# Optimization experiments

Measured on AMD Instinct MI355X. Metric: run time of the kernel, lower is better.

Reference implementation:

```python
import jax, jax.numpy as jnp
import numpy as np

TIME_LAG, PRE_LEN, STATIONS, SAMPLES = 12, 3, 40, 38
B, H, DM, DFF = 4, 8, 512, 2048
L = STATIONS * SAMPLES          # 1520 tokens fed to Informer
SAMPLE_K = 40                   # factor(5)*ceil(ln L); also n_top selected queries
N_ENC = 2


def sinusoid(length, d):
    pos = np.arange(length, dtype=np.float32)[:, None]
    i = np.arange(d)[None, :]
    ang = pos / np.power(10000.0, (2 * (i // 2)) / d)
    pe = np.where(i % 2 == 0, np.sin(ang), np.cos(ang)).astype(np.float32)
    return jnp.asarray(pe)


def layernorm(x, g, b, eps=1e-5):
    mu = x.mean(-1, keepdims=True)
    var = ((x - mu) ** 2).mean(-1, keepdims=True)
    return (x - mu) * jax.lax.rsqrt(var + eps) * g + b


def heads(x):
    b, l, d = x.shape
    return x.reshape(b, l, H, d // H).transpose(0, 2, 1, 3)


def unheads(x):
    b, h, l, dh = x.shape
    return x.transpose(0, 2, 1, 3).reshape(b, l, h * dh)


def prob_attention(Q, K, V, idx):
    # ProbSparse attention (Informer). Q,K,V: [B,H,L,Dh]; idx: [L, SAMPLE_K] sampled key ids.
    b, h, l, dh = Q.shape
    def col(ic):  # one sampled key per query; avoids [B,H,L,S,Dh] gather blowup
        return jnp.einsum('bhld,bhld->bhl', Q, K[:, :, ic, :])
    qk_s = jnp.moveaxis(jax.lax.map(col, idx.T), 0, -1)       # [B,H,L,SAMPLE_K]
    M = qk_s.max(-1) - qk_s.sum(-1) / l                        # sparsity measure
    _, top = jax.lax.top_k(M, SAMPLE_K)                        # [B,H,n_top]
    Qr = jnp.take_along_axis(Q, top[..., None], axis=2)        # [B,H,n_top,Dh]
    scores = jnp.einsum('bhud,bhkd->bhuk', Qr, K) / jnp.sqrt(jnp.float32(dh))
    ctx_top = jax.nn.softmax(scores, axis=-1) @ V              # [B,H,n_top,Dh]
    ctx = jnp.broadcast_to(V.mean(axis=2, keepdims=True), Q.shape)
    bi = jnp.arange(b)[:, None, None]
    hi = jnp.arange(h)[None, :, None]
    return ctx.at[bi, hi, top].set(ctx_top)


def full_attention(Q, K, V):
    scores = jnp.einsum('bhqd,bhkd->bhqk', Q, K) / jnp.sqrt(jnp.float32(Q.shape[-1]))
    return jax.nn.softmax(scores, axis=-1) @ V


def ffn(x, Wa, ba, Wb, bb):
    return jax.nn.gelu(x @ Wa + ba) @ Wb + bb


def _forward(inflow, P, samp_idx):
    x = inflow[:, 2:2 + TIME_LAG].reshape(B, -1, TIME_LAG)     # [B,L,T] (row-major, same as torch)
    pe = sinusoid(L, DM)
    enc = x @ P['W_emb_e'] + P['b_emb_e'] + pe
    for i in range(N_ENC):
        qkv = enc @ P['enc_Wqkv'][i] + P['enc_bqkv'][i]
        q, k, v = jnp.split(qkv, 3, axis=-1)
        ctx = unheads(prob_attention(heads(q), heads(k), heads(v), samp_idx[i]))
        enc = layernorm(enc + ctx @ P['enc_Wo'][i] + P['enc_bo'][i], P['enc_ln1_g'][i], P['enc_ln1_b'][i])
        y = ffn(enc, P['enc_Wf1'][i], P['enc_bf1'][i], P['enc_Wf2'][i], P['enc_bf2'][i])
        enc = layernorm(enc + y, P['enc_ln2_g'][i], P['enc_ln2_b'][i])
    enc = layernorm(enc, P['enc_norm_g'], P['enc_norm_b'])
    dec = x @ P['W_emb_d'] + P['b_emb_d'] + pe
    qkv = dec @ P['dec_Wqkv'] + P['dec_bqkv']
    q, k, v = jnp.split(qkv, 3, axis=-1)
    ctx = unheads(prob_attention(heads(q), heads(k), heads(v), samp_idx[2]))
    dec = layernorm(dec + ctx @ P['dec_Wo_s'] + P['dec_bo_s'], P['dec_ln1_g'], P['dec_ln1_b'])
    qc = dec @ P['dec_Wq_c'] + P['dec_bq_c']
    kc, vc = jnp.split(enc @ P['dec_Wkv_c'] + P['dec_bkv_c'], 2, axis=-1)
    ctx = unheads(full_attention(heads(qc), heads(kc), heads(vc)))
    dec = layernorm(dec + ctx @ P['dec_Wo_c'] + P['dec_bo_c'], P['dec_ln2_g'], P['dec_ln2_b'])
    y = ffn(dec, P['dec_Wf1'], P['dec_bf1'], P['dec_Wf2'], P['dec_bf2'])
    dec = layernorm(dec + y, P['dec_ln3_g'], P['dec_ln3_b'])
    out = dec @ P['W_proj'] + P['b_proj'] + x                  # Informer output + residual
    out = jax.nn.relu(out @ P['W1'] + P['b1']) @ P['W3'] + P['b3']
    return out.reshape(B, PRE_LEN, STATIONS, SAMPLES)


def setup_inputs():
    key = jax.random.key(0)
    keys = iter(jax.random.split(key, 80))
    def w(*shape):
        return jax.random.normal(next(keys), shape, jnp.float32) * 0.02
    def zeros(*shape):
        return jnp.zeros(shape, jnp.float32)
    def ones(*shape):
        return jnp.ones(shape, jnp.float32)
    inp = dict(
        flow=zeros(1), ODRate=zeros(1), adj=zeros(1), external=zeros(1),
        inflow=jax.random.normal(next(keys), (B, 2 + TIME_LAG, STATIONS, SAMPLES), jnp.float32),
        W_emb_e=w(TIME_LAG, DM), b_emb_e=zeros(DM),
        W_emb_d=w(TIME_LAG, DM), b_emb_d=zeros(DM),
        enc_Wqkv=w(N_ENC, DM, 3 * DM), enc_bqkv=zeros(N_ENC, 3 * DM),
        enc_Wo=w(N_ENC, DM, DM), enc_bo=zeros(N_ENC, DM),
        enc_ln1_g=ones(N_ENC, DM), enc_ln1_b=zeros(N_ENC, DM),
        enc_Wf1=w(N_ENC, DM, DFF), enc_bf1=zeros(N_ENC, DFF),
        enc_Wf2=w(N_ENC, DFF, DM), enc_bf2=zeros(N_ENC, DM),
        enc_ln2_g=ones(N_ENC, DM), enc_ln2_b=zeros(N_ENC, DM),
        enc_norm_g=ones(DM), enc_norm_b=zeros(DM),
        dec_Wqkv=w(DM, 3 * DM), dec_bqkv=zeros(3 * DM),
        dec_Wo_s=w(DM, DM), dec_bo_s=zeros(DM),
        dec_ln1_g=ones(DM), dec_ln1_b=zeros(DM),
        dec_Wq_c=w(DM, DM), dec_bq_c=zeros(DM),
        dec_Wkv_c=w(DM, 2 * DM), dec_bkv_c=zeros(2 * DM),
        dec_Wo_c=w(DM, DM), dec_bo_c=zeros(DM),
        dec_ln2_g=ones(DM), dec_ln2_b=zeros(DM),
        dec_Wf1=w(DM, DFF), dec_bf1=zeros(DFF),
        dec_Wf2=w(DFF, DM), dec_bf2=zeros(DM),
        dec_ln3_g=ones(DM), dec_ln3_b=zeros(DM),
        W_proj=w(DM, TIME_LAG), b_proj=zeros(TIME_LAG),
        W1=w(TIME_LAG, 128), b1=zeros(128),
        W3=w(128, PRE_LEN), b3=zeros(PRE_LEN),
        samp_idx=jax.random.randint(next(keys), (3, L, SAMPLE_K), 0, L, jnp.int32),
    )
    return inp


def reference(flow, inflow, ODRate, adj, external, W_emb_e, b_emb_e, W_emb_d, b_emb_d, enc_Wqkv, enc_bqkv, enc_Wo, enc_bo, enc_ln1_g, enc_ln1_b, enc_Wf1, enc_bf1, enc_Wf2, enc_bf2, enc_ln2_g, enc_ln2_b, enc_norm_g, enc_norm_b, dec_Wqkv, dec_bqkv, dec_Wo_s, dec_bo_s, dec_ln1_g, dec_ln1_b, dec_Wq_c, dec_bq_c, dec_Wkv_c, dec_bkv_c, dec_Wo_c, dec_bo_c, dec_ln2_g, dec_ln2_b, dec_Wf1, dec_bf1, dec_Wf2, dec_bf2, dec_ln3_g, dec_ln3_b, W_proj, b_proj, W1, b1, W3, b3, samp_idx):
    args = locals()
    skip = ('flow', 'inflow', 'ODRate', 'adj', 'external', 'samp_idx')
    P = {k: v for k, v in args.items() if k not in skip}
    return _forward(inflow, P, samp_idx)
```

## Files before the change

kernel.cpp:

```cpp
#include <hip/hip_runtime.h>
#include <math.h>

#define B_ 4
#define H_ 8
#define L_ 1520
#define DM_ 512
#define DFF_ 2048
#define SK_ 40
#define ML_ (B_*L_)
#define MP_ 6144
#define LP_ 1536

typedef unsigned short u16;
typedef short s8v __attribute__((ext_vector_type(8)));
typedef float f4 __attribute__((ext_vector_type(4)));

__device__ __forceinline__ u16 f2b(float x) {
  union { float f; unsigned u; } c; c.f = x;
  unsigned r = c.u + 0x7FFFu + ((c.u >> 16) & 1u);
  return (u16)(r >> 16);
}
__device__ __forceinline__ float b2f(u16 h) {
  union { unsigned u; float f; } c; c.u = ((unsigned)h) << 16;
  return c.f;
}
__device__ __forceinline__ float gelu_tanh(float x) {
  float x3 = x * x * x;
  return 0.5f * x * (1.f + tanhf(0.79788456080286536f * (x + 0.044715f * x3)));
}
__device__ __forceinline__ int xswz(int bid, int cpx) {
  return (bid & 7) * cpx + (bid >> 3);
}

__global__ __launch_bounds__(256) void pe_kernel(float* __restrict__ pe) {
  int idx = blockIdx.x * 256 + threadIdx.x;
  if (idx >= L_ * DM_) return;
  int pos = idx / DM_, i = idx % DM_;
  double expo = (double)(2 * (i / 2)) / (double)DM_;
  double ang = (double)pos / pow(10000.0, expo);
  pe[idx] = (i & 1) ? (float)cos(ang) : (float)sin(ang);
}

__global__ __launch_bounds__(256) void extract_x(const float* __restrict__ inflow,
                                                 float* __restrict__ X) {
  int idx = blockIdx.x * 256 + threadIdx.x;
  if (idx >= ML_ * 12) return;
  int b = idx / (L_ * 12);
  int rem = idx - b * (L_ * 12);
  X[idx] = inflow[(size_t)b * 14 * L_ + 2 * L_ + rem];
}

struct CvtArgs {
  const float* src[15];
  unsigned cum[16];
  unsigned lk[15];
};
__global__ __launch_bounds__(256) void cvt_all(CvtArgs a, u16* __restrict__ dst) {
  unsigned idx = blockIdx.x * 256 + threadIdx.x;
  int s = 0;
#pragma unroll
  for (int i = 1; i < 15; ++i) s += (idx >= a.cum[i]);
  unsigned local = idx - a.cum[s];
  unsigned lk = a.lk[s];
  unsigned K = 1u << lk;
  unsigned N = (a.cum[s + 1] - a.cum[s]) >> lk;
  unsigned n = local >> lk, k = local & (K - 1);
  dst[idx] = f2b(a.src[s][(size_t)k * N + n]);
}

__global__ __launch_bounds__(256) void embed_fused(
    const float* __restrict__ X, const float* __restrict__ W,
    const float* __restrict__ bias, const float* __restrict__ PE,
    float* __restrict__ ACT, u16* __restrict__ ACTb) {
  int row = blockIdx.x * 4 + (threadIdx.x >> 6);
  int lane = threadIdx.x & 63;
  int d0 = lane * 8;
  if (row >= ML_) {
    s8v z = {0, 0, 0, 0, 0, 0, 0, 0};
    *(s8v*)(ACTb + (size_t)row * DM_ + d0) = z;
    return;
  }
  int prow = row % L_;
  f4 a0 = *(const f4*)(bias + d0);
  f4 a1 = *(const f4*)(bias + d0 + 4);
  a0 += *(const f4*)(PE + (size_t)prow * DM_ + d0);
  a1 += *(const f4*)(PE + (size_t)prow * DM_ + d0 + 4);
  const float* xr = X + (size_t)row * 12;
#pragma unroll
  for (int t = 0; t < 12; ++t) {
    float xv = xr[t];
    a0 += xv * *(const f4*)(W + (size_t)t * DM_ + d0);
    a1 += xv * *(const f4*)(W + (size_t)t * DM_ + d0 + 4);
  }
  float* dst = ACT + (size_t)row * DM_ + d0;
  *(f4*)dst = a0;
  *(f4*)(dst + 4) = a1;
  u16 ob[8];
#pragma unroll
  for (int i = 0; i < 4; ++i) { ob[i] = f2b(a0[i]); ob[4 + i] = f2b(a1[i]); }
  *(s8v*)(ACTb + (size_t)row * DM_ + d0) = *(s8v*)ob;
}

__global__ __launch_bounds__(256) void head_fused(
    const float* __restrict__ DEC, const float* __restrict__ X,
    const float* __restrict__ Wp, const float* __restrict__ bp,
    const float* __restrict__ W1, const float* __restrict__ b1,
    const float* __restrict__ W3, const float* __restrict__ b3,
    float* __restrict__ out) {
  int row = blockIdx.x * 4 + (threadIdx.x >> 6);
  int lane = threadIdx.x & 63;
  int d0 = lane * 8;
  const float* dec = DEC + (size_t)row * DM_ + d0;
  f4 v0 = *(const f4*)dec;
  f4 v1 = *(const f4*)(dec + 4);
  float pj[12];
#pragma unroll
  for (int j = 0; j < 12; ++j) pj[j] = 0.f;
#pragma unroll
  for (int i = 0; i < 8; ++i) {
    float dv = (i < 4) ? v0[i] : v1[i - 4];
    const float* wr = Wp + (size_t)(d0 + i) * 12;
#pragma unroll
    for (int j = 0; j < 12; ++j) pj[j] += dv * wr[j];
  }
  for (int off = 32; off; off >>= 1) {
#pragma unroll
    for (int j = 0; j < 12; ++j) pj[j] += __shfl_xor(pj[j], off);
  }
  float o12[12];
#pragma unroll
  for (int j = 0; j < 12; ++j) o12[j] = pj[j] + bp[j] + X[(size_t)row * 12 + j];
  int k0 = lane * 2;
  float h0 = b1[k0], h1 = b1[k0 + 1];
#pragma unroll
  for (int j = 0; j < 12; ++j) {
    h0 += o12[j] * W1[j * 128 + k0];
    h1 += o12[j] * W1[j * 128 + k0 + 1];
  }
  h0 = fmaxf(h0, 0.f);
  h1 = fmaxf(h1, 0.f);
  float op[3];
#pragma unroll
  for (int p = 0; p < 3; ++p)
    op[p] = h0 * W3[k0 * 3 + p] + h1 * W3[(k0 + 1) * 3 + p];
  for (int off = 32; off; off >>= 1) {
#pragma unroll
    for (int p = 0; p < 3; ++p) op[p] += __shfl_xor(op[p], off);
  }
  if (lane == 0) {
#pragma unroll
    for (int p = 0; p < 3; ++p) out[(size_t)row * 3 + p] = op[p] + b3[p];
  }
}

template<int BM>
__global__ __launch_bounds__(256) void gemm_bf16(
    const u16* __restrict__ A, const u16* __restrict__ Bt,
    const float* __restrict__ bias, const float* __restrict__ res,
    float* __restrict__ Cf, u16* __restrict__ Cb,
    int N, int K, int act) {
  __shared__ __align__(16) u16 As[BM * 32];
  __shared__ __align__(16) u16 Bs[128 * 32];
  constexpr int MI = BM / 32;
  const int nwg = gridDim.x * gridDim.y;
  const int lin = blockIdx.y * gridDim.x + blockIdx.x;
  const int o = xswz(lin, nwg >> 3);
  const int bxi = o % gridDim.x, byi = o / gridDim.x;
  const int t = threadIdx.x, w = t >> 6, lane = t & 63;
  const int lg = lane >> 4, li = lane & 15;
  const int bm = byi * BM, bn = bxi * 128;
  const int wr = (w >> 1) * (BM / 2), wc = (w & 1) * 64;
  f4 acc[MI][4];
#pragma unroll
  for (int i = 0; i < MI; ++i)
#pragma unroll
    for (int j = 0; j < 4; ++j) acc[i][j] = f4{0.f, 0.f, 0.f, 0.f};
  const int rB = w * 32 + (lane >> 2);
  const int rA = (BM == 128) ? rB : (w * 16 + (lane >> 2));
  const int ps = lane & 3;
  for (int k0 = 0; k0 < K; k0 += 32) {
    if (BM == 128) {
#pragma unroll
      for (int j = 0; j < 2; ++j) {
        int r = rA + j * 16;
        int ls = ps ^ ((r >> 1) & 3);
        __builtin_amdgcn_global_load_lds(
            (const __attribute__((address_space(1))) void*)(A + (size_t)(bm + r) * K + k0 + ls * 8),
            (__attribute__((address_space(3))) void*)(As + (w * 32 + j * 16) * 32),
            16, 0, 0);
      }
    } else {
      int ls = ps ^ ((rA >> 1) & 3);
      __builtin_amdgcn_global_load_lds(
          (const __attribute__((address_space(1))) void*)(A + (size_t)(bm + rA) * K + k0 + ls * 8),
          (__attribute__((address_space(3))) void*)(As + (w * 16) * 32),
          16, 0, 0);
    }
#pragma unroll
    for (int j = 0; j < 2; ++j) {
      int r = rB + j * 16;
      int ls = ps ^ ((r >> 1) & 3);
      __builtin_amdgcn_global_load_lds(
          (const __attribute__((address_space(1))) void*)(Bt + (size_t)(bn + r) * K + k0 + ls * 8),
          (__attribute__((address_space(3))) void*)(Bs + (w * 32 + j * 16) * 32),
          16, 0, 0);
    }
    __syncthreads();
    s8v af[MI], bf[4];
#pragma unroll
    for (int f = 0; f < MI; ++f) {
      int ra = wr + f * 16 + li;
      af[f] = *(const s8v*)(As + ra * 32 + ((lg ^ ((ra >> 1) & 3)) * 8));
    }
#pragma unroll
    for (int f = 0; f < 4; ++f) {
      int rb = wc + f * 16 + li;
      bf[f] = *(const s8v*)(Bs + rb * 32 + ((lg ^ ((rb >> 1) & 3)) * 8));
    }
#pragma unroll
    for (int fi = 0; fi < MI; ++fi)
#pragma unroll
      for (int fj = 0; fj < 4; ++fj)
        acc[fi][fj] = __builtin_amdgcn_mfma_f32_16x16x32_bf16(af[fi], bf[fj], acc[fi][fj], 0, 0, 0);
    __syncthreads();
  }
#pragma unroll
  for (int fi = 0; fi < MI; ++fi)
#pragma unroll
    for (int fj = 0; fj < 4; ++fj)
#pragma unroll
      for (int r = 0; r < 4; ++r) {
        int row = bm + wr + fi * 16 + lg * 4 + r;
        int col = bn + wc + fj * 16 + li;
        float v = acc[fi][fj][r] + bias[col];
        if (res && row < ML_) v += res[(size_t)row * N + col];
        if (act == 1) v = gelu_tanh(v);
        if (Cf && row < ML_) Cf[(size_t)row * N + col] = v;
        if (Cb) Cb[(size_t)row * N + col] = f2b(v);
      }
}

__global__ __launch_bounds__(256) void layernorm_ip(float* __restrict__ Xb,
                                                    const float* __restrict__ g,
                                                    const float* __restrict__ bta,
                                                    u16* __restrict__ outb) {
  int row = blockIdx.x * 4 + (threadIdx.x >> 6);
  int lane = threadIdx.x & 63;
  float* x = Xb + (size_t)row * DM_;
  f4 a = *(f4*)(x + lane * 8);
  f4 b = *(f4*)(x + lane * 8 + 4);
  float s = a[0] + a[1] + a[2] + a[3] + b[0] + b[1] + b[2] + b[3];
  for (int off = 32; off; off >>= 1) s += __shfl_xor(s, off);
  float mu = s * (1.f / 512.f);
  float vs = 0.f;
#pragma unroll
  for (int i = 0; i < 4; ++i) { a[i] -= mu; b[i] -= mu; vs += a[i] * a[i] + b[i] * b[i]; }
  for (int off = 32; off; off >>= 1) vs += __shfl_xor(vs, off);
  float rs = rsqrtf(vs * (1.f / 512.f) + 1e-5f);
  f4 g0 = *(const f4*)(g + lane * 8), g1 = *(const f4*)(g + lane * 8 + 4);
  f4 c0 = *(const f4*)(bta + lane * 8), c1 = *(const f4*)(bta + lane * 8 + 4);
  u16 ob[8];
#pragma unroll
  for (int i = 0; i < 4; ++i) {
    float r1 = a[i] * rs * g0[i] + c0[i]; x[lane * 8 + i] = r1;     ob[i] = f2b(r1);
    float r2 = b[i] * rs * g1[i] + c1[i]; x[lane * 8 + 4 + i] = r2; ob[4 + i] = f2b(r2);
  }
  *(s8v*)(outb + (size_t)row * DM_ + lane * 8) = *(s8v*)ob;
}

__global__ __launch_bounds__(256) void probM(const u16* __restrict__ qkv,
                                             const int* __restrict__ sidx,
                                             float* __restrict__ Mout) {
  int wid = threadIdx.x / 64, lane = threadIdx.x % 64;
  int o = xswz(blockIdx.x, (B_ * H_ * L_ / 4) >> 3);
  int g = o * 4 + wid;
  int l = g % L_;
  int bh = g / L_;
  int h = bh % H_, b = bh / H_;
  __shared__ float qs[4][64];
  qs[wid][lane] = b2f(qkv[((size_t)b * L_ + l) * 1536 + h * 64 + lane]);
  __syncthreads();
  float dot = 0.f;
  if (lane < SK_) {
    int ks = sidx[l * SK_ + lane];
    const u16* kr = qkv + ((size_t)b * L_ + ks) * 1536 + 512 + h * 64;
#pragma unroll
    for (int j = 0; j < 8; ++j) {
      s8v v = *(const s8v*)(kr + j * 8);
#pragma unroll
      for (int i = 0; i < 8; ++i) dot += qs[wid][j * 8 + i] * b2f((u16)v[i]);
    }
  }
  float vmax = (lane < SK_) ? dot : -INFINITY;
  float vsum = (lane < SK_) ? dot : 0.f;
  for (int off = 32; off; off >>= 1) {
    vmax = fmaxf(vmax, __shfl_xor(vmax, off));
    vsum += __shfl_xor(vsum, off);
  }
  if (lane == 0) Mout[g] = vmax - vsum / (float)L_;
}

__global__ __launch_bounds__(256) void radix_topk(const float* __restrict__ Mv,
                                                  int* __restrict__ top) {
  const int bh = blockIdx.x;
  const int t = threadIdx.x;
  const int base = t * 6;
  unsigned key[6];
#pragma unroll
  for (int i = 0; i < 6; ++i) {
    int ix = base + i;
    unsigned k = 0u;
    if (ix < L_) {
      union { float f; unsigned u; } c; c.f = Mv[(size_t)bh * L_ + ix];
      k = c.u ^ ((c.u & 0x80000000u) ? 0xFFFFFFFFu : 0x80000000u);
    }
    key[i] = k;
  }
  __shared__ int wred[4];
  __shared__ int s_a[256], s_b[256];
  unsigned prefix = 0u;
  for (int b = 31; b >= 0; --b) {
    unsigned cand = prefix | (1u << b);
    int c = 0;
#pragma unroll
    for (int i = 0; i < 6; ++i) c += (key[i] >= cand);
    for (int off = 32; off; off >>= 1) c += __shfl_xor(c, off);
    if ((t & 63) == 0) wred[t >> 6] = c;
    __syncthreads();
    int tot = wred[0] + wred[1] + wred[2] + wred[3];
    if (tot >= SK_) prefix = cand;
    __syncthreads();
  }
  const unsigned T = prefix;
  int gt = 0, tie = 0;
#pragma unroll
  for (int i = 0; i < 6; ++i) { gt += (key[i] > T); tie += (key[i] == T); }
  s_a[t] = gt; s_b[t] = tie;
  __syncthreads();
  for (int off = 1; off < 256; off <<= 1) {
    int va = (t >= off) ? s_a[t - off] : 0;
    int vb = (t >= off) ? s_b[t - off] : 0;
    __syncthreads();
    s_a[t] += va; s_b[t] += vb;
    __syncthreads();
  }
  const int n_strict = s_a[255];
  const int gt_base = s_a[t] - gt;
  const int tie_base = s_b[t] - tie;
  const int need = SK_ - n_strict;
  int lgt = 0, ltie = 0;
#pragma unroll
  for (int i = 0; i < 6; ++i) {
    int ix = base + i;
    if (key[i] > T) {
      top[bh * SK_ + gt_base + lgt] = ix; ++lgt;
    } else if (key[i] == T) {
      int r = tie_base + ltie; ++ltie;
      if (r < need) top[bh * SK_ + n_strict + r] = ix;
    }
  }
}

__global__ __launch_bounds__(256) void transpose_v(const u16* __restrict__ src,
                                                   int stride, int voff0,
                                                   u16* __restrict__ VT) {
  int o = xswz(blockIdx.x, (B_ * H_ * 24) >> 3);
  int kt = o % 24, bh = o / 24;
  int h = bh & 7, b = bh >> 3;
  int kb = kt * 64;
  __shared__ u16 tile[64][72];
  int t = threadIdx.x;
#pragma unroll
  for (int rr = 0; rr < 2; ++rr) {
    int slot = rr * 256 + t;
    int key = slot >> 3, d = (slot & 7) * 8;
    int gk = kb + key; if (gk >= L_) gk = L_ - 1;
    s8v v = *(const s8v*)(src + (size_t)(b * L_ + gk) * stride + voff0 + h * 64 + d);
    *(s8v*)(&tile[key][d]) = v;
  }
  __syncthreads();
  int dim = t >> 2, k0 = (t & 3) * 16;
  u16 buf[16];
#pragma unroll
  for (int i = 0; i < 16; ++i) {
    int key = k0 + i;
    buf[i] = (kb + key < L_) ? tile[key][dim] : (u16)0;
  }
  *(s8v*)(VT + ((size_t)bh * 64 + dim) * LP_ + kb + k0) = *(s8v*)buf;
  *(s8v*)(VT + ((size_t)bh * 64 + dim) * LP_ + kb + k0 + 8) = *(s8v*)(buf + 8);
}

template<int MODE>
__global__ __launch_bounds__(256) void flash_attn(
    const u16* __restrict__ Qm, const u16* __restrict__ Kg,
    const u16* __restrict__ VT, const int* __restrict__ top,
    float* __restrict__ POf, u16* POa, u16* POb,
    float* __restrict__ PM, float* __restrict__ PL) {
  constexpr int QSTR = (MODE == 0) ? 512 : 1536;
  constexpr int KSTR = (MODE == 0) ? 512 : 1536;
  constexpr int TILES = (MODE == 0) ? 12 : 3;
  constexpr int NB = (MODE == 0) ? 48 : 8;
  __shared__ __align__(16) u16 Kt[64 * 64];
  __shared__ __align__(16) u16 Vt[64 * 64];
  __shared__ __align__(16) unsigned Xch[4][576];
  const int o = xswz(blockIdx.x, (B_ * H_ * NB) >> 3);
  int bh, sp, qb;
  if (MODE == 0) {
    bh = o / 48; int rem = o % 48; qb = rem >> 1; sp = rem & 1;
  } else {
    bh = o / 8; sp = o % 8; qb = 0;
  }
  const int h = bh & 7, b = bh >> 3;
  const int qoff = h * 64;
  const int koff = ((MODE == 0) ? 0 : 512) + h * 64;
  const int t = threadIdx.x, w = t >> 6, lane = t & 63;
  const int lg = lane >> 4, li = lane & 15;
  const u16* vtg = VT + (size_t)bh * 64 * LP_;
  unsigned* xw = Xch[w];
  u16* xw16 = (u16*)xw;

  int qrow;
  if (MODE == 0) {
    int q = qb * 64 + w * 16 + li;
    qrow = b * L_ + ((q < L_) ? q : (L_ - 1));
  } else {
    int u = w * 16 + li; if (u >= SK_) u = SK_ - 1;
    qrow = b * L_ + top[bh * SK_ + u];
  }
  s8v qf0 = *(const s8v*)(Qm + (size_t)qrow * QSTR + qoff + lg * 8);
  s8v qf1 = *(const s8v*)(Qm + (size_t)qrow * QSTR + qoff + 32 + lg * 8);

  f4 o4[4];
#pragma unroll
  for (int n = 0; n < 4; ++n) o4[n] = f4{0.f, 0.f, 0.f, 0.f};
  float m_run = -INFINITY, l_run = 0.f;
  const int kt0 = sp * TILES;
  const int skey = lane >> 3;
  const int sslot = lane & 7;

#pragma unroll 1
  for (int ki = 0; ki < TILES; ++ki) {
    const int kb = (kt0 + ki) * 64;
#pragma unroll
    for (int j = 0; j < 2; ++j) {
      int row = w * 16 + j * 8 + skey;
      int gk = kb + row; if (gk >= L_) gk = L_ - 1;
      int ck = sslot ^ (row & 7);
      __builtin_amdgcn_global_load_lds(
          (const __attribute__((address_space(1))) void*)(Kg + (size_t)(b * L_ + gk) * KSTR + koff + ck * 8),
          (__attribute__((address_space(3))) void*)(Kt + (w * 16 + j * 8) * 64),
          16, 0, 0);
      int cv = sslot ^ (row & 7);
      __builtin_amdgcn_global_load_lds(
          (const __attribute__((address_space(1))) void*)(vtg + (size_t)row * LP_ + kb + cv * 8),
          (__attribute__((address_space(3))) void*)(Vt + (w * 16 + j * 8) * 64),
          16, 0, 0);
    }
    __syncthreads();
    f4 s[4];
#pragma unroll
    for (int c = 0; c < 4; ++c) {
      int key = c * 16 + li;
      s8v kf = *(const s8v*)(Kt + key * 64 + ((lg ^ (key & 7)) * 8));
      s8v kg2 = *(const s8v*)(Kt + key * 64 + (((lg + 4) ^ (key & 7)) * 8));
      f4 z = f4{0.f, 0.f, 0.f, 0.f};
      z = __builtin_amdgcn_mfma_f32_16x16x32_bf16(kf, qf0, z, 0, 0, 0);
      z = __builtin_amdgcn_mfma_f32_16x16x32_bf16(kg2, qf1, z, 0, 0, 0);
      s[c] = z * 0.125f;
    }
    if (kb + 64 > L_) {
#pragma unroll
      for (int c = 0; c < 4; ++c)
#pragma unroll
        for (int r = 0; r < 4; ++r)
          if (kb + c * 16 + lg * 4 + r >= L_) s[c][r] = -INFINITY;
    }
    float tm = -INFINITY;
#pragma unroll
    for (int c = 0; c < 4; ++c)
      tm = fmaxf(tm, fmaxf(fmaxf(s[c][0], s[c][1]), fmaxf(s[c][2], s[c][3])));
    tm = fmaxf(tm, __shfl_xor(tm, 16));
    tm = fmaxf(tm, __shfl_xor(tm, 32));
    float mn = fmaxf(m_run, tm);
    float sc = __expf(m_run - mn);
    float p[4][4];
    float rs = 0.f;
#pragma unroll
    for (int c = 0; c < 4; ++c)
#pragma unroll
      for (int r = 0; r < 4; ++r) { p[c][r] = __expf(s[c][r] - mn); rs += p[c][r]; }
    rs += __shfl_xor(rs, 16);
    rs += __shfl_xor(rs, 32);
    l_run = l_run * sc + rs;
    m_run = mn;
#pragma unroll
    for (int n = 0; n < 4; ++n) o4[n] *= sc;
#pragma unroll
    for (int c = 0; c < 4; ++c)
#pragma unroll
      for (int rp = 0; rp < 2; ++rp) {
        unsigned v = (unsigned)f2b(p[c][2 * rp]) | ((unsigned)f2b(p[c][2 * rp + 1]) << 16);
        xw[li * 36 + c * 8 + lg * 2 + rp] = v;
      }
    s8v pb0 = *(const s8v*)(xw + li * 36 + lg * 4);
    s8v pb1 = *(const s8v*)(xw + li * 36 + 16 + lg * 4);
#pragma unroll
    for (int n = 0; n < 4; ++n) {
      int dim = n * 16 + li;
      s8v vb0 = *(const s8v*)(Vt + dim * 64 + ((lg ^ (dim & 7)) * 8));
      o4[n] = __builtin_amdgcn_mfma_f32_16x16x32_bf16(vb0, pb0, o4[n], 0, 0, 0);
    }
#pragma unroll
    for (int n = 0; n < 4; ++n) {
      int dim = n * 16 + li;
      s8v vb1 = *(const s8v*)(Vt + dim * 64 + (((lg + 4) ^ (dim & 7)) * 8));
      o4[n] = __builtin_amdgcn_mfma_f32_16x16x32_bf16(vb1, pb1, o4[n], 0, 0, 0);
    }
    __syncthreads();
  }

  if (MODE == 0) {
#pragma unroll
    for (int n = 0; n < 4; ++n)
#pragma unroll
      for (int r = 0; r < 4; ++r)
        xw16[li * 72 + n * 16 + lg * 4 + r] = f2b(o4[n][r]);
    u16* PO = sp ? POb : POa;
    const int pid = (bh * 24 + qb) * 2 + sp;
    int q_local = lane >> 2, d0 = (lane & 3) * 16;
    int q = qb * 64 + w * 16 + q_local;
    s8v v0 = *(const s8v*)(xw16 + q_local * 72 + d0);
    s8v v1 = *(const s8v*)(xw16 + q_local * 72 + d0 + 8);
    if (q < L_) {
      u16* dst = PO + ((size_t)(b * L_ + q)) * DM_ + qoff + d0;
      *(s8v*)dst = v0;
      *(s8v*)(dst + 8) = v1;
    }
    if (lg == 0) {
      PM[pid * 64 + w * 16 + li] = m_run;
      PL[pid * 64 + w * 16 + li] = l_run;
    }
  } else {
    int base = (bh * 8 + sp) * 64 + w * 16 + li;
#pragma unroll
    for (int n = 0; n < 4; ++n)
#pragma unroll
      for (int r = 0; r < 4; ++r)
        POf[(size_t)base * 64 + n * 16 + lg * 4 + r] = o4[n][r];
    if (lg == 0) {
      PM[base] = m_run;
      PL[base] = l_run;
    }
  }
}

__global__ __launch_bounds__(256) void combine_cross(const u16* __restrict__ PO0,
                                                     const float* __restrict__ PM,
                                                     const float* __restrict__ PL,
                                                     u16* ctxb) {
  int idx = blockIdx.x * 256 + threadIdx.x;
  int row = idx >> 9, col = idx & 511;
  int b = row / L_, q = row - b * L_;
  int h = col >> 6;
  int bh = b * 8 + h, qbk = q >> 6, qi = q & 63;
  int p0 = ((bh * 24 + qbk) * 2) * 64 + qi;
  float m0 = PM[p0], m1 = PM[p0 + 64];
  float l0 = PL[p0], l1 = PL[p0 + 64];
  float M = fmaxf(m0, m1);
  float w0 = __expf(m0 - M), w1 = __expf(m1 - M);
  float inv = 1.f / (w0 * l0 + w1 * l1);
  float o0 = b2f(PO0[idx]);
  float o1 = b2f(ctxb[idx]);
  ctxb[idx] = f2b((w0 * o0 + w1 * o1) * inv);
}

__global__ __launch_bounds__(256) void combine_prob(const float* __restrict__ PO,
                                                    const float* __restrict__ PM,
                                                    const float* __restrict__ PL,
                                                    float* __restrict__ ctt) {
  int bh = blockIdx.x;
  int t = threadIdx.x;
  int u = t >> 2, dg = (t & 3) * 16;
  if (u >= SK_) return;
  float M = -INFINITY;
  for (int s = 0; s < 8; ++s) M = fmaxf(M, PM[(bh * 8 + s) * 64 + u]);
  float wgt[8];
  float den = 0.f;
  for (int s = 0; s < 8; ++s) {
    wgt[s] = __expf(PM[(bh * 8 + s) * 64 + u] - M);
    den += wgt[s] * PL[(bh * 8 + s) * 64 + u];
  }
  float inv = 1.f / den;
  for (int d = dg; d < dg + 16; ++d) {
    float acc = 0.f;
    for (int s = 0; s < 8; ++s) acc += wgt[s] * PO[(((size_t)bh * 8 + s) * 64 + u) * 64 + d];
    ctt[((size_t)bh * SK_ + u) * 64 + d] = acc * inv;
  }
}

__global__ __launch_bounds__(256) void vmean_part(const u16* __restrict__ qkv,
                                                  float* __restrict__ part) {
  int g = xswz(blockIdx.x, (B_ * H_ * 8) >> 3);
  int bh = g >> 3, seg = g & 7;
  int h = bh & 7, b = bh >> 3;
  int lane = threadIdx.x & 63, grp = threadIdx.x >> 6;
  int k0 = seg * 190, k1 = k0 + 190;
  float acc = 0.f;
  for (int k = k0 + grp; k < k1; k += 4)
    acc += b2f(qkv[((size_t)b * L_ + k) * 1536 + 1024 + h * 64 + lane]);
  __shared__ float pv[4][64];
  pv[grp][lane] = acc;
  __syncthreads();
  if (threadIdx.x < 64)
    part[g * 64 + threadIdx.x] =
        pv[0][threadIdx.x] + pv[1][threadIdx.x] + pv[2][threadIdx.x] + pv[3][threadIdx.x];
}

__global__ __launch_bounds__(256) void vmean_comb(const float* __restrict__ part,
                                                  float* __restrict__ vmean) {
  int idx = blockIdx.x * 256 + threadIdx.x;
  int bh = idx >> 6, d = idx & 63;
  float s = 0.f;
#pragma unroll
  for (int seg = 0; seg < 8; ++seg) s += part[(bh * 8 + seg) * 64 + d];
  vmean[idx] = s / (float)L_;
}

__global__ __launch_bounds__(256) void fill_ctx(const float* __restrict__ vmean,
                                                u16* __restrict__ ctxb) {
  int idx = blockIdx.x * 256 + threadIdx.x;
  int d = idx % 64;
  int h = (idx / 64) % H_;
  int b = idx / (L_ * DM_);
  ctxb[idx] = f2b(vmean[(b * H_ + h) * 64 + d]);
}

__global__ __launch_bounds__(256) void scatter_ctx(const float* __restrict__ ctt,
                                                   const int* __restrict__ top,
                                                   u16* __restrict__ ctxb) {
  int idx = blockIdx.x * 256 + threadIdx.x;
  int d = idx % 64;
  int u = (idx / 64) % SK_;
  int bh = idx / (64 * SK_);
  int h = bh % H_, b = bh / H_;
  int l = top[bh * SK_ + u];
  ctxb[((size_t)b * L_ + l) * DM_ + h * 64 + d] = f2b(ctt[idx]);
}

extern "C" void kernel_launch(void* const* d_in, const int* in_sizes, int n_in,
                              void* d_out, int out_size, void* d_ws, size_t ws_size,
                              hipStream_t stream) {
  const float* inflow   = (const float*)d_in[4];
  const float* W_emb_e  = (const float*)d_in[5];
  const float* b_emb_e  = (const float*)d_in[6];
  const float* W_emb_d  = (const float*)d_in[7];
  const float* b_emb_d  = (const float*)d_in[8];
  const float* enc_Wqkv = (const float*)d_in[9];
  const float* enc_bqkv = (const float*)d_in[10];
  const float* enc_Wo   = (const float*)d_in[11];
  const float* enc_bo   = (const float*)d_in[12];
  const float* enc_ln1g = (const float*)d_in[13];
  const float* enc_ln1b = (const float*)d_in[14];
  const float* enc_Wf1  = (const float*)d_in[15];
  const float* enc_bf1  = (const float*)d_in[16];
  const float* enc_Wf2  = (const float*)d_in[17];
  const float* enc_bf2  = (const float*)d_in[18];
  const float* enc_ln2g = (const float*)d_in[19];
  const float* enc_ln2b = (const float*)d_in[20];
  const float* enc_ng   = (const float*)d_in[21];
  const float* enc_nb   = (const float*)d_in[22];
  const float* dec_Wqkv = (const float*)d_in[23];
  const float* dec_bqkv = (const float*)d_in[24];
  const float* dec_Wo_s = (const float*)d_in[25];
  const float* dec_bo_s = (const float*)d_in[26];
  const float* dec_ln1g = (const float*)d_in[27];
  const float* dec_ln1b = (const float*)d_in[28];
  const float* dec_Wq_c = (const float*)d_in[29];
  const float* dec_bq_c = (const float*)d_in[30];
  const float* dec_Wkv  = (const float*)d_in[31];
  const float* dec_bkv  = (const float*)d_in[32];
  const float* dec_Wo_c = (const float*)d_in[33];
  const float* dec_bo_c = (const float*)d_in[34];
  const float* dec_ln2g = (const float*)d_in[35];
  const float* dec_ln2b = (const float*)d_in[36];
  const float* dec_Wf1  = (const float*)d_in[37];
  const float* dec_bf1  = (const float*)d_in[38];
  const float* dec_Wf2  = (const float*)d_in[39];
  const float* dec_bf2  = (const float*)d_in[40];
  const float* dec_ln3g = (const float*)d_in[41];
  const float* dec_ln3b = (const float*)d_in[42];
  const float* W_proj   = (const float*)d_in[43];
  const float* b_proj   = (const float*)d_in[44];
  const float* W1       = (const float*)d_in[45];
  const float* b1       = (const float*)d_in[46];
  const float* W3       = (const float*)d_in[47];
  const float* b3       = (const float*)d_in[48];
  const int*   samp     = (const int*)d_in[49];
  float* out = (float*)d_out;

  float* ws  = (float*)d_ws;
  float* PE  = ws;
  float* X   = PE + 778240;
  float* ACT = X + 72960;
  float* REG = ACT + 3112960;
  float* MME = REG + 6291456;
  float* CTT = MME + 48640;
  float* VME = CTT + 81920;
  int*   TOP = (int*)(VME + 2048);
  float* TAIL = VME + 2048 + 1280;
  u16* ENCb = (u16*)TAIL;
  u16* DECb = (u16*)(TAIL + 1572864);
  u16* CTXb = (u16*)(TAIL + 2 * 1572864);
  u16* WBF  = (u16*)(TAIL + 3 * 1572864);

  u16* QKVb = (u16*)REG;
  u16* FFb  = (u16*)REG;
  u16* VT   = (u16*)REG + 9437184;
  u16* QCb  = (u16*)REG;
  u16* Kc   = (u16*)REG + 3145728;
  u16* Vc   = (u16*)REG + 6291456;
  float* POp = (float*)CTXb;
  float* PMp = POp + 1048576;
  float* PLp = PMp + 16384;
  float* PMc = PE;
  float* PLc = PE + 98304;
  float* VME8 = MME;

  auto GB = [&](const u16* A, const u16* Bt, const float* bias, const float* res,
                float* Cf, u16* Cb, int N, int K, int act) {
    if (N <= 512) {
      dim3 g(N / 128, MP_ / 64);
      gemm_bf16<64><<<g, 256, 0, stream>>>(A, Bt, bias, res, Cf, Cb, N, K, act);
    } else {
      dim3 g(N / 128, MP_ / 128);
      gemm_bf16<128><<<g, 256, 0, stream>>>(A, Bt, bias, res, Cf, Cb, N, K, act);
    }
  };
  auto PROB = [&](const int* sidx) {
    probM<<<B_ * H_ * L_ / 4, 256, 0, stream>>>(QKVb, sidx, MME);
    radix_topk<<<B_ * H_, 256, 0, stream>>>(MME, TOP);
    transpose_v<<<B_ * H_ * 24, 256, 0, stream>>>(QKVb, 1536, 1024, VT);
    flash_attn<1><<<B_ * H_ * 8, 256, 0, stream>>>(QKVb, QKVb, VT, TOP, POp,
                                                   nullptr, nullptr, PMp, PLp);
    combine_prob<<<B_ * H_, 256, 0, stream>>>(POp, PMp, PLp, CTT);
    vmean_part<<<B_ * H_ * 8, 256, 0, stream>>>(QKVb, VME8);
    vmean_comb<<<8, 256, 0, stream>>>(VME8, VME);
    fill_ctx<<<ML_ * DM_ / 256, 256, 0, stream>>>(VME, CTXb);
    scatter_ctx<<<B_ * H_ * SK_ * 64 / 256, 256, 0, stream>>>(CTT, TOP, CTXb);
  };

  pe_kernel<<<(L_ * DM_ + 255) / 256, 256, 0, stream>>>(PE);
  extract_x<<<(ML_ * 12 + 255) / 256, 256, 0, stream>>>(inflow, X);

  {
    CvtArgs a;
    const float* s[15] = {
      enc_Wqkv, enc_Wqkv + 512 * 1536, enc_Wo, enc_Wo + 512 * 512,
      enc_Wf1, enc_Wf1 + 512 * 2048, enc_Wf2, enc_Wf2 + 2048 * 512,
      dec_Wqkv, dec_Wo_s, dec_Wq_c, dec_Wkv, dec_Wo_c, dec_Wf1, dec_Wf2 };
    unsigned cum[16] = { 0u, 786432u, 1572864u, 1835008u, 2097152u, 3145728u,
                         4194304u, 5242880u, 6291456u, 7077888u, 7340032u,
                         7602176u, 8126464u, 8388608u, 9437184u, 10485760u };
    unsigned lk[15] = { 9, 9, 9, 9, 9, 9, 11, 11, 9, 9, 9, 9, 9, 9, 11 };
    for (int i = 0; i < 15; ++i) { a.src[i] = s[i]; a.lk[i] = lk[i]; }
    for (int i = 0; i < 16; ++i) a.cum[i] = cum[i];
    cvt_all<<<10485760 / 256, 256, 0, stream>>>(a, WBF);
  }
  u16* Wt_qkv_e0 = WBF + 0;
  u16* Wt_qkv_e1 = WBF + 786432;
  u16* Wt_o_e0   = WBF + 1572864;
  u16* Wt_o_e1   = WBF + 1835008;
  u16* Wt_f1_e0  = WBF + 2097152;
  u16* Wt_f1_e1  = WBF + 3145728;
  u16* Wt_f2_e0  = WBF + 4194304;
  u16* Wt_f2_e1  = WBF + 5242880;
  u16* Wt_qkv_d  = WBF + 6291456;
  u16* Wt_o_s    = WBF + 7077888;
  u16* Wt_q_c    = WBF + 7340032;
  u16* Wt_kv_c   = WBF + 7602176;
  u16* Wt_o_c    = WBF + 8126464;
  u16* Wt_f1_d   = WBF + 8388608;
  u16* Wt_f2_d   = WBF + 9437184;

  embed_fused<<<MP_ / 4, 256, 0, stream>>>(X, W_emb_e, b_emb_e, PE, ACT, ENCb);

  const u16* Wqkv_e[2] = {Wt_qkv_e0, Wt_qkv_e1};
  const u16* Wo_e[2]   = {Wt_o_e0, Wt_o_e1};
  const u16* Wf1_e[2]  = {Wt_f1_e0, Wt_f1_e1};
  const u16* Wf2_e[2]  = {Wt_f2_e0, Wt_f2_e1};
  for (int i = 0; i < 2; ++i) {
    GB(ENCb, Wqkv_e[i], enc_bqkv + i * 1536, nullptr, nullptr, QKVb, 1536, 512, 0);
    PROB(samp + (size_t)i * L_ * SK_);
    GB(CTXb, Wo_e[i], enc_bo + i * 512, ACT, ACT, nullptr, 512, 512, 0);
    layernorm_ip<<<ML_ / 4, 256, 0, stream>>>(ACT, enc_ln1g + i * 512, enc_ln1b + i * 512, ENCb);
    GB(ENCb, Wf1_e[i], enc_bf1 + i * 2048, nullptr, nullptr, FFb, 2048, 512, 1);
    GB(FFb, Wf2_e[i], enc_bf2 + i * 512, ACT, ACT, nullptr, 512, 2048, 0);
    layernorm_ip<<<ML_ / 4, 256, 0, stream>>>(ACT, enc_ln2g + i * 512, enc_ln2b + i * 512, ENCb);
  }
  layernorm_ip<<<ML_ / 4, 256, 0, stream>>>(ACT, enc_ng, enc_nb, ENCb);

  embed_fused<<<MP_ / 4, 256, 0, stream>>>(X, W_emb_d, b_emb_d, PE, ACT, DECb);
  GB(DECb, Wt_qkv_d, dec_bqkv, nullptr, nullptr, QKVb, 1536, 512, 0);
  PROB(samp + (size_t)2 * L_ * SK_);
  GB(CTXb, Wt_o_s, dec_bo_s, ACT, ACT, nullptr, 512, 512, 0);
  layernorm_ip<<<ML_ / 4, 256, 0, stream>>>(ACT, dec_ln1g, dec_ln1b, DECb);

  GB(DECb, Wt_q_c, dec_bq_c, nullptr, nullptr, QCb, 512, 512, 0);
  GB(ENCb, Wt_kv_c, dec_bkv, nullptr, nullptr, Kc, 512, 512, 0);
  GB(ENCb, Wt_kv_c + 512 * 512, dec_bkv + 512, nullptr, nullptr, Vc, 512, 512, 0);
  transpose_v<<<B_ * H_ * 24, 256, 0, stream>>>(Vc, 512, 0, VT);
  flash_attn<0><<<B_ * H_ * 48, 256, 0, stream>>>(QCb, Kc, VT, nullptr, nullptr,
                                                  Vc, CTXb, PMc, PLc);
  combine_cross<<<ML_ * DM_ / 256, 256, 0, stream>>>(Vc, PMc, PLc, CTXb);
  GB(CTXb, Wt_o_c, dec_bo_c, ACT, ACT, nullptr, 512, 512, 0);
  layernorm_ip<<<ML_ / 4, 256, 0, stream>>>(ACT, dec_ln2g, dec_ln2b, DECb);

  GB(DECb, Wt_f1_d, dec_bf1, nullptr, nullptr, FFb, 2048, 512, 1);
  GB(FFb, Wt_f2_d, dec_bf2, ACT, ACT, nullptr, 512, 2048, 0);
  layernorm_ip<<<ML_ / 4, 256, 0, stream>>>(ACT, dec_ln3g, dec_ln3b, DECb);

  head_fused<<<ML_ / 4, 256, 0, stream>>>(ACT, X, W_proj, b_proj, W1, b1, W3, b3, out);
}
```

Baseline: 918.9 us.

## Double-buffer GEMM LDS tiles and tile-transpose weight conversion through shared memory

The bf16 GEMM now keeps two LDS buffers per operand and issues the global-to-LDS loads for the next K slice before the MFMAs on the current one, which removes one barrier per iteration and overlaps load latency with compute. The weight fp32-to-bf16 transpose kernel now works on 32x32 tiles staged in padded shared memory, so both the strided reads and the writes are coalesced instead of gathering with a large stride. The cost is double the LDS footprint in the GEMM, which may lower occupancy.

New measurement: 1.045 ms. 13.7% more time.

```diff
diff --git a/kernel.cpp b/kernel.cpp
--- a/kernel.cpp
+++ b/kernel.cpp
@@ -52,20 +52,31 @@
 
 struct CvtArgs {
   const float* src[15];
-  unsigned cum[16];
+  unsigned cumt[16];
   unsigned lk[15];
 };
 __global__ __launch_bounds__(256) void cvt_all(CvtArgs a, u16* __restrict__ dst) {
-  unsigned idx = blockIdx.x * 256 + threadIdx.x;
+  __shared__ float tl[32][33];
+  int bt = blockIdx.x;
   int s = 0;
 #pragma unroll
-  for (int i = 1; i < 15; ++i) s += (idx >= a.cum[i]);
-  unsigned local = idx - a.cum[s];
+  for (int i = 1; i < 15; ++i) s += (bt >= (int)a.cumt[i]);
+  int lt = bt - a.cumt[s];
   unsigned lk = a.lk[s];
   unsigned K = 1u << lk;
-  unsigned N = (a.cum[s + 1] - a.cum[s]) >> lk;
-  unsigned n = local >> lk, k = local & (K - 1);
-  dst[idx] = f2b(a.src[s][(size_t)k * N + n]);
+  unsigned N = ((a.cumt[s + 1] - a.cumt[s]) << 10) >> lk;
+  unsigned tiles_n = N >> 5;
+  unsigned k0 = (lt / tiles_n) * 32, n0 = (lt % tiles_n) * 32;
+  const float* src = a.src[s];
+  int r = threadIdx.x >> 5, c = threadIdx.x & 31;
+#pragma unroll
+  for (int i = 0; i < 4; ++i)
+    tl[r + 8 * i][c] = src[(size_t)(k0 + r + 8 * i) * N + n0 + c];
+  __syncthreads();
+  u16* d = dst + ((size_t)a.cumt[s] << 10);
+#pragma unroll
+  for (int i = 0; i < 4; ++i)
+    d[(size_t)(n0 + r + 8 * i) * K + k0 + c] = f2b(tl[c][r + 8 * i]);
 }
 
 __global__ __launch_bounds__(256) void embed_fused(
@@ -159,8 +170,8 @@
     const float* __restrict__ bias, const float* __restrict__ res,
     float* __restrict__ Cf, u16* __restrict__ Cb,
     int N, int K, int act) {
-  __shared__ __align__(16) u16 As[BM * 32];
-  __shared__ __align__(16) u16 Bs[128 * 32];
+  __shared__ __align__(16) u16 As[2][BM * 32];
+  __shared__ __align__(16) u16 Bs[2][128 * 32];
   constexpr int MI = BM / 32;
   const int nwg = gridDim.x * gridDim.y;
   const int lin = blockIdx.y * gridDim.x + blockIdx.x;
@@ -178,7 +189,8 @@
   const int rB = w * 32 + (lane >> 2);
   const int rA = (BM == 128) ? rB : (w * 16 + (lane >> 2));
   const int ps = lane & 3;
-  for (int k0 = 0; k0 < K; k0 += 32) {
+
+  auto STAGE = [&](int bf, int k0) {
     if (BM == 128) {
 #pragma unroll
       for (int j = 0; j < 2; ++j) {
@@ -186,14 +198,14 @@
         int ls = ps ^ ((r >> 1) & 3);
         __builtin_amdgcn_global_load_lds(
             (const __attribute__((address_space(1))) void*)(A + (size_t)(bm + r) * K + k0 + ls * 8),
-            (__attribute__((address_space(3))) void*)(As + (w * 32 + j * 16) * 32),
+            (__attribute__((address_space(3))) void*)(&As[bf][(w * 32 + j * 16) * 32]),
             16, 0, 0);
       }
     } else {
       int ls = ps ^ ((rA >> 1) & 3);
       __builtin_amdgcn_global_load_lds(
           (const __attribute__((address_space(1))) void*)(A + (size_t)(bm + rA) * K + k0 + ls * 8),
-          (__attribute__((address_space(3))) void*)(As + (w * 16) * 32),
+          (__attribute__((address_space(3))) void*)(&As[bf][(w * 16) * 32]),
           16, 0, 0);
     }
 #pragma unroll
@@ -202,27 +214,35 @@
       int ls = ps ^ ((r >> 1) & 3);
       __builtin_amdgcn_global_load_lds(
           (const __attribute__((address_space(1))) void*)(Bt + (size_t)(bn + r) * K + k0 + ls * 8),
-          (__attribute__((address_space(3))) void*)(Bs + (w * 32 + j * 16) * 32),
+          (__attribute__((address_space(3))) void*)(&Bs[bf][(w * 32 + j * 16) * 32]),
           16, 0, 0);
     }
-    __syncthreads();
+  };
+
+  STAGE(0, 0);
+  __syncthreads();
+  int cur = 0;
+  for (int k0 = 0; k0 < K; k0 += 32) {
+    const bool has_next = (k0 + 32 < K);
+    if (has_next) STAGE(cur ^ 1, k0 + 32);
     s8v af[MI], bf[4];
 #pragma unroll
     for (int f = 0; f < MI; ++f) {
       int ra = wr + f * 16 + li;
-      af[f] = *(const s8v*)(As + ra * 32 + ((lg ^ ((ra >> 1) & 3)) * 8));
+      af[f] = *(const s8v*)(&As[cur][ra * 32 + ((lg ^ ((ra >> 1) & 3)) * 8)]);
     }
 #pragma unroll
     for (int f = 0; f < 4; ++f) {
       int rb = wc + f * 16 + li;
-      bf[f] = *(const s8v*)(Bs + rb * 32 + ((lg ^ ((rb >> 1) & 3)) * 8));
+      bf[f] = *(const s8v*)(&Bs[cur][rb * 32 + ((lg ^ ((rb >> 1) & 3)) * 8)]);
     }
 #pragma unroll
     for (int fi = 0; fi < MI; ++fi)
 #pragma unroll
       for (int fj = 0; fj < 4; ++fj)
         acc[fi][fj] = __builtin_amdgcn_mfma_f32_16x16x32_bf16(af[fi], bf[fj], acc[fi][fj], 0, 0, 0);
-    __syncthreads();
+    if (has_next) __syncthreads();
+    cur ^= 1;
   }
 #pragma unroll
   for (int fi = 0; fi < MI; ++fi)
@@ -758,13 +778,13 @@
       enc_Wqkv, enc_Wqkv + 512 * 1536, enc_Wo, enc_Wo + 512 * 512,
       enc_Wf1, enc_Wf1 + 512 * 2048, enc_Wf2, enc_Wf2 + 2048 * 512,
       dec_Wqkv, dec_Wo_s, dec_Wq_c, dec_Wkv, dec_Wo_c, dec_Wf1, dec_Wf2 };
-    unsigned cum[16] = { 0u, 786432u, 1572864u, 1835008u, 2097152u, 3145728u,
-                         4194304u, 5242880u, 6291456u, 7077888u, 7340032u,
-                         7602176u, 8126464u, 8388608u, 9437184u, 10485760u };
+    unsigned cumt[16] = { 0u, 768u, 1536u, 1792u, 2048u, 3072u,
+                          4096u, 5120u, 6144u, 6912u, 7168u,
+                          7424u, 7936u, 8192u, 9216u, 10240u };
     unsigned lk[15] = { 9, 9, 9, 9, 9, 9, 11, 11, 9, 9, 9, 9, 9, 9, 11 };
     for (int i = 0; i < 15; ++i) { a.src[i] = s[i]; a.lk[i] = lk[i]; }
-    for (int i = 0; i < 16; ++i) a.cum[i] = cum[i];
-    cvt_all<<<10485760 / 256, 256, 0, stream>>>(a, WBF);
+    for (int i = 0; i < 16; ++i) a.cumt[i] = cumt[i];
+    cvt_all<<<10240, 256, 0, stream>>>(a, WBF);
   }
   u16* Wt_qkv_e0 = WBF + 0;
   u16* Wt_qkv_e1 = WBF + 786432;
```
